# Optimization experiments

Hardware: AMD Instinct MI355X
Metric: run time of the kernel (lower is better)

## Reference

```python
import jax, jax.numpy as jnp
import numpy as np

B, N1, NL, D_MODEL, A, D_K, D_V, D_OUT = 16, 32, 256, 16, 2, 8, 8, 16


def setup_inputs() -> dict:
    key = jax.random.key(0)
    ks = jax.random.split(key, 7)
    he = lambda k, shape, fan_in: jax.random.normal(k, shape, dtype=jnp.float32) * np.sqrt(2.0 / fan_in).astype(np.float32)
    return {
        "Q": jax.random.normal(ks[0], (B, N1, NL, D_MODEL), dtype=jnp.float32),
        "K": jax.random.normal(ks[1], (B, N1, NL, D_MODEL), dtype=jnp.float32),
        "V": jax.random.normal(ks[2], (B, N1, NL, D_MODEL), dtype=jnp.float32),
        "Wq": he(ks[3], (D_MODEL, A, D_K), D_MODEL),
        "Wk": he(ks[4], (D_MODEL, A, D_K), D_MODEL),
        "Wv": he(ks[5], (D_MODEL, A, D_V), D_MODEL),
        "Wo": he(ks[6], (D_V, A, D_OUT), D_V),
    }


def reference(Q, K, V, Wq, Wk, Wv, Wo):
    # Per-head projections: [B, N1, NL, D_k|D_v, A]
    Qp = jnp.einsum('bnki,iaj->bnkja', Q, Wq)
    Kp = jnp.einsum('bnki,iaj->bnkja', K, Wk)
    Vp = jnp.einsum('bnki,iaj->bnkja', V, Wv)
    # Attention maps: [B, N1, NL, NL, A], elementwise ReLU instead of softmax
    attn = jnp.einsum('bnkja,bnzja->bnkza', Qp, Kp)
    attn = jax.nn.relu(attn)
    # Weighted sum of values: [B, N1, NL, D_v, A]
    emb = jnp.einsum('bnkza,bnzma->bnkma', attn, Vp)
    # Output projection mixing heads: [B, N1, NL, D_out]
    proj = jnp.einsum('bnkma,maz->bnkz', emb, Wo)
    # Mean attention map over heads: [B, N1, NL, NL]
    attn_mean = jnp.mean(attn, axis=-1)
    return (proj, attn_mean)
```

## Files before the change

### kernel.cpp

```cpp
#include <hip/hip_runtime.h>

#define B_    16
#define N1_   32
#define NL_   256
#define DM_   16
#define A_    2
#define DK_   8
#define DV_   8
#define DOUT_ 16

#define NBN   (B_ * N1_)
#define PROJ_ELEMS (NBN * NL_ * DOUT_)
#define ZT    32
#define ATP   33

__global__ __launch_bounds__(256, 2)
void mha_relu_kernel(const float* __restrict__ Q,
                     const float* __restrict__ K,
                     const float* __restrict__ V,
                     const float* __restrict__ Wq,
                     const float* __restrict__ Wk,
                     const float* __restrict__ Wv,
                     const float* __restrict__ Wo,
                     float* __restrict__ proj_out,
                     float* __restrict__ attn_out)
{
    __shared__ float sWq[DM_ * A_ * DK_];
    __shared__ float sWk[DM_ * A_ * DK_];
    __shared__ float sWv[DM_ * A_ * DV_];
    __shared__ float sWo[DV_ * A_ * DOUT_];
    __shared__ float KP[NL_ * 16];
    __shared__ float VP[NL_ * 16];
    __shared__ float AT[NL_ * ATP];

    const int tid = threadIdx.x;
    const int bn  = blockIdx.x;
    const int k   = tid;

    sWq[tid] = Wq[tid];
    sWk[tid] = Wk[tid];
    sWv[tid] = Wv[tid];
    sWo[tid] = Wo[tid];
    __syncthreads();

    const size_t inoff = (size_t)bn * NL_ * DM_;

    float Qp[16];
    float rowbuf[16];

    {
        const float4* p = (const float4*)(Q + inoff + (size_t)k * DM_);
        #pragma unroll
        for (int i = 0; i < 4; ++i) {
            float4 t = p[i];
            rowbuf[4*i+0] = t.x; rowbuf[4*i+1] = t.y;
            rowbuf[4*i+2] = t.z; rowbuf[4*i+3] = t.w;
        }
        #pragma unroll
        for (int t = 0; t < 16; ++t) Qp[t] = 0.f;
        #pragma unroll
        for (int i = 0; i < 16; ++i) {
            float qi = rowbuf[i];
            #pragma unroll
            for (int t = 0; t < 16; ++t) Qp[t] += qi * sWq[i*16 + t];
        }
    }
    {
        const float4* p = (const float4*)(K + inoff + (size_t)k * DM_);
        #pragma unroll
        for (int i = 0; i < 4; ++i) {
            float4 t = p[i];
            rowbuf[4*i+0] = t.x; rowbuf[4*i+1] = t.y;
            rowbuf[4*i+2] = t.z; rowbuf[4*i+3] = t.w;
        }
        float acc[16];
        #pragma unroll
        for (int t = 0; t < 16; ++t) acc[t] = 0.f;
        #pragma unroll
        for (int i = 0; i < 16; ++i) {
            float ki = rowbuf[i];
            #pragma unroll
            for (int t = 0; t < 16; ++t) acc[t] += ki * sWk[i*16 + t];
        }
        #pragma unroll
        for (int t = 0; t < 16; ++t) KP[k*16 + t] = acc[t];
    }
    {
        const float4* p = (const float4*)(V + inoff + (size_t)k * DM_);
        #pragma unroll
        for (int i = 0; i < 4; ++i) {
            float4 t = p[i];
            rowbuf[4*i+0] = t.x; rowbuf[4*i+1] = t.y;
            rowbuf[4*i+2] = t.z; rowbuf[4*i+3] = t.w;
        }
        float acc[16];
        #pragma unroll
        for (int t = 0; t < 16; ++t) acc[t] = 0.f;
        #pragma unroll
        for (int i = 0; i < 16; ++i) {
            float vi = rowbuf[i];
            #pragma unroll
            for (int t = 0; t < 16; ++t) acc[t] += vi * sWv[i*16 + t];
        }
        #pragma unroll
        for (int t = 0; t < 16; ++t) VP[k*16 + t] = acc[t];
    }
    __syncthreads();

    float emb[16];
    #pragma unroll
    for (int t = 0; t < 16; ++t) emb[t] = 0.f;

    float* atrow = &AT[k * ATP];
    float* aout  = attn_out + (size_t)bn * NL_ * NL_;

    for (int tile = 0; tile < NL_ / ZT; ++tile) {
        const int z0 = tile * ZT;

        #pragma unroll 8
        for (int zt = 0; zt < ZT; ++zt) {
            const int z = z0 + zt;
            const float4* kpv = (const float4*)&KP[z * 16];
            float kp[16];
            #pragma unroll
            for (int i = 0; i < 4; ++i) {
                float4 t = kpv[i];
                kp[4*i+0] = t.x; kp[4*i+1] = t.y;
                kp[4*i+2] = t.z; kp[4*i+3] = t.w;
            }
            float s0 = 0.f, s1 = 0.f;
            #pragma unroll
            for (int j = 0; j < 8; ++j) {
                s0 += Qp[j]     * kp[j];
                s1 += Qp[8 + j] * kp[8 + j];
            }
            s0 = fmaxf(s0, 0.f);
            s1 = fmaxf(s1, 0.f);
            atrow[zt] = 0.5f * (s0 + s1);

            const float4* vpv = (const float4*)&VP[z * 16];
            float vp[16];
            #pragma unroll
            for (int i = 0; i < 4; ++i) {
                float4 t = vpv[i];
                vp[4*i+0] = t.x; vp[4*i+1] = t.y;
                vp[4*i+2] = t.z; vp[4*i+3] = t.w;
            }
            #pragma unroll
            for (int t = 0; t < 8; ++t) {
                emb[t]     += s0 * vp[t];
                emb[8 + t] += s1 * vp[8 + t];
            }
        }
        __syncthreads();

        #pragma unroll
        for (int i = 0; i < (NL_ * ZT) / 256; ++i) {
            const int idx = i * 256 + tid;
            const int row = idx >> 5;
            const int col = idx & 31;
            aout[(size_t)row * NL_ + z0 + col] = AT[row * ATP + col];
        }
        __syncthreads();
    }

    float pr[16];
    #pragma unroll
    for (int o = 0; o < 16; ++o) pr[o] = 0.f;
    #pragma unroll
    for (int a = 0; a < 2; ++a) {
        #pragma unroll
        for (int m = 0; m < 8; ++m) {
            const float e = emb[a*8 + m];
            #pragma unroll
            for (int o = 0; o < 16; ++o) pr[o] += e * sWo[m*32 + a*16 + o];
        }
    }
    float4* po = (float4*)(proj_out + (size_t)bn * NL_ * DOUT_ + (size_t)k * DOUT_);
    po[0] = make_float4(pr[0],  pr[1],  pr[2],  pr[3]);
    po[1] = make_float4(pr[4],  pr[5],  pr[6],  pr[7]);
    po[2] = make_float4(pr[8],  pr[9],  pr[10], pr[11]);
    po[3] = make_float4(pr[12], pr[13], pr[14], pr[15]);
}

extern "C" void kernel_launch(void* const* d_in, const int* in_sizes, int n_in,
                              void* d_out, int out_size, void* d_ws, size_t ws_size,
                              hipStream_t stream) {
    const float* Q  = (const float*)d_in[0];
    const float* K  = (const float*)d_in[1];
    const float* V  = (const float*)d_in[2];
    const float* Wq = (const float*)d_in[3];
    const float* Wk = (const float*)d_in[4];
    const float* Wv = (const float*)d_in[5];
    const float* Wo = (const float*)d_in[6];

    float* proj = (float*)d_out;
    float* attn = (float*)d_out + PROJ_ELEMS;

    mha_relu_kernel<<<NBN, 256, 0, stream>>>(Q, K, V, Wq, Wk, Wv, Wo, proj, attn);
}
```

Measured before the change: 75.91 us.

## Register-tile four query rows per thread and split key range across waves

Each wave now owns a 64-key slice and each thread computes four query rows, so every K/V row read from LDS is reused four times instead of once. Attention-map values are written straight to global memory as float4, replacing the LDS transpose tile and its per-tile barriers. Partial embeddings from the four waves are reduced through LDS before the output projection. This costs more registers (64 Qp plus 64 emb accumulators per thread) and adds a cross-wave reduction. Each thread's float4 stores now land at addresses a full row apart, so they coalesce less well than before.

```diff
diff --git a/kernel.cpp b/kernel.cpp
--- a/kernel.cpp
+++ b/kernel.cpp
@@ -11,8 +11,17 @@
 
 #define NBN   (B_ * N1_)
 #define PROJ_ELEMS (NBN * NL_ * DOUT_)
-#define ZT    32
-#define ATP   33
+
+#define QP_OFF   0
+#define KP_OFF   4352
+#define VP_OFF   8448
+#define WQ_OFF   12544
+#define WK_OFF   12800
+#define WV_OFF   13056
+#define WO_OFF   13312
+#define LDS_FLOATS 13568
+#define EMBA_OFF 0
+#define EMBB_OFF 4352
 
 __global__ __launch_bounds__(256, 2)
 void mha_relu_kernel(const float* __restrict__ Q,
@@ -25,144 +34,167 @@
                      float* __restrict__ proj_out,
                      float* __restrict__ attn_out)
 {
-    __shared__ float sWq[DM_ * A_ * DK_];
-    __shared__ float sWk[DM_ * A_ * DK_];
-    __shared__ float sWv[DM_ * A_ * DV_];
-    __shared__ float sWo[DV_ * A_ * DOUT_];
-    __shared__ float KP[NL_ * 16];
-    __shared__ float VP[NL_ * 16];
-    __shared__ float AT[NL_ * ATP];
+    __shared__ float lds[LDS_FLOATS];
 
     const int tid = threadIdx.x;
     const int bn  = blockIdx.x;
-    const int k   = tid;
-
-    sWq[tid] = Wq[tid];
-    sWk[tid] = Wk[tid];
-    sWv[tid] = Wv[tid];
-    sWo[tid] = Wo[tid];
+    const int w   = tid >> 6;
+    const int l   = tid & 63;
+
+    lds[WQ_OFF + tid] = Wq[tid];
+    lds[WK_OFF + tid] = Wk[tid];
+    lds[WV_OFF + tid] = Wv[tid];
+    lds[WO_OFF + tid] = Wo[tid];
     __syncthreads();
 
     const size_t inoff = (size_t)bn * NL_ * DM_;
 
-    float Qp[16];
-    float rowbuf[16];
-
     {
-        const float4* p = (const float4*)(Q + inoff + (size_t)k * DM_);
-        #pragma unroll
-        for (int i = 0; i < 4; ++i) {
-            float4 t = p[i];
-            rowbuf[4*i+0] = t.x; rowbuf[4*i+1] = t.y;
-            rowbuf[4*i+2] = t.z; rowbuf[4*i+3] = t.w;
-        }
-        #pragma unroll
-        for (int t = 0; t < 16; ++t) Qp[t] = 0.f;
-        #pragma unroll
-        for (int i = 0; i < 16; ++i) {
-            float qi = rowbuf[i];
-            #pragma unroll
-            for (int t = 0; t < 16; ++t) Qp[t] += qi * sWq[i*16 + t];
-        }
-    }
-    {
-        const float4* p = (const float4*)(K + inoff + (size_t)k * DM_);
-        #pragma unroll
-        for (int i = 0; i < 4; ++i) {
-            float4 t = p[i];
-            rowbuf[4*i+0] = t.x; rowbuf[4*i+1] = t.y;
-            rowbuf[4*i+2] = t.z; rowbuf[4*i+3] = t.w;
-        }
-        float acc[16];
-        #pragma unroll
-        for (int t = 0; t < 16; ++t) acc[t] = 0.f;
-        #pragma unroll
-        for (int i = 0; i < 16; ++i) {
-            float ki = rowbuf[i];
-            #pragma unroll
-            for (int t = 0; t < 16; ++t) acc[t] += ki * sWk[i*16 + t];
-        }
-        #pragma unroll
-        for (int t = 0; t < 16; ++t) KP[k*16 + t] = acc[t];
-    }
-    {
-        const float4* p = (const float4*)(V + inoff + (size_t)k * DM_);
-        #pragma unroll
-        for (int i = 0; i < 4; ++i) {
-            float4 t = p[i];
-            rowbuf[4*i+0] = t.x; rowbuf[4*i+1] = t.y;
-            rowbuf[4*i+2] = t.z; rowbuf[4*i+3] = t.w;
-        }
-        float acc[16];
-        #pragma unroll
-        for (int t = 0; t < 16; ++t) acc[t] = 0.f;
-        #pragma unroll
-        for (int i = 0; i < 16; ++i) {
-            float vi = rowbuf[i];
-            #pragma unroll
-            for (int t = 0; t < 16; ++t) acc[t] += vi * sWv[i*16 + t];
-        }
-        #pragma unroll
-        for (int t = 0; t < 16; ++t) VP[k*16 + t] = acc[t];
-    }
-    __syncthreads();
-
-    float emb[16];
-    #pragma unroll
-    for (int t = 0; t < 16; ++t) emb[t] = 0.f;
-
-    float* atrow = &AT[k * ATP];
-    float* aout  = attn_out + (size_t)bn * NL_ * NL_;
-
-    for (int tile = 0; tile < NL_ / ZT; ++tile) {
-        const int z0 = tile * ZT;
-
-        #pragma unroll 8
-        for (int zt = 0; zt < ZT; ++zt) {
-            const int z = z0 + zt;
-            const float4* kpv = (const float4*)&KP[z * 16];
-            float kp[16];
+        float rowbuf[16], acc[16];
+
+        {
+            const float4* p = (const float4*)(Q + inoff + (size_t)tid * DM_);
             #pragma unroll
             for (int i = 0; i < 4; ++i) {
-                float4 t = kpv[i];
-                kp[4*i+0] = t.x; kp[4*i+1] = t.y;
-                kp[4*i+2] = t.z; kp[4*i+3] = t.w;
-            }
-            float s0 = 0.f, s1 = 0.f;
-            #pragma unroll
-            for (int j = 0; j < 8; ++j) {
-                s0 += Qp[j]     * kp[j];
-                s1 += Qp[8 + j] * kp[8 + j];
-            }
-            s0 = fmaxf(s0, 0.f);
-            s1 = fmaxf(s1, 0.f);
-            atrow[zt] = 0.5f * (s0 + s1);
-
-            const float4* vpv = (const float4*)&VP[z * 16];
-            float vp[16];
+                float4 t = p[i];
+                rowbuf[4*i+0] = t.x; rowbuf[4*i+1] = t.y;
+                rowbuf[4*i+2] = t.z; rowbuf[4*i+3] = t.w;
+            }
+            #pragma unroll
+            for (int c = 0; c < 16; ++c) acc[c] = 0.f;
+            #pragma unroll
+            for (int i = 0; i < 16; ++i) {
+                const float qi = rowbuf[i];
+                #pragma unroll
+                for (int c = 0; c < 16; ++c) acc[c] += qi * lds[WQ_OFF + i*16 + c];
+            }
+            #pragma unroll
+            for (int c = 0; c < 16; ++c) lds[QP_OFF + tid*17 + c] = acc[c];
+        }
+        {
+            const float4* p = (const float4*)(K + inoff + (size_t)tid * DM_);
             #pragma unroll
             for (int i = 0; i < 4; ++i) {
-                float4 t = vpv[i];
-                vp[4*i+0] = t.x; vp[4*i+1] = t.y;
-                vp[4*i+2] = t.z; vp[4*i+3] = t.w;
-            }
-            #pragma unroll
-            for (int t = 0; t < 8; ++t) {
-                emb[t]     += s0 * vp[t];
-                emb[8 + t] += s1 * vp[8 + t];
-            }
-        }
-        __syncthreads();
-
-        #pragma unroll
-        for (int i = 0; i < (NL_ * ZT) / 256; ++i) {
-            const int idx = i * 256 + tid;
-            const int row = idx >> 5;
-            const int col = idx & 31;
-            aout[(size_t)row * NL_ + z0 + col] = AT[row * ATP + col];
-        }
-        __syncthreads();
-    }
+                float4 t = p[i];
+                rowbuf[4*i+0] = t.x; rowbuf[4*i+1] = t.y;
+                rowbuf[4*i+2] = t.z; rowbuf[4*i+3] = t.w;
+            }
+            #pragma unroll
+            for (int c = 0; c < 16; ++c) acc[c] = 0.f;
+            #pragma unroll
+            for (int i = 0; i < 16; ++i) {
+                const float ki = rowbuf[i];
+                #pragma unroll
+                for (int c = 0; c < 16; ++c) acc[c] += ki * lds[WK_OFF + i*16 + c];
+            }
+            #pragma unroll
+            for (int c = 0; c < 16; ++c) lds[KP_OFF + tid*16 + c] = acc[c];
+        }
+        {
+            const float4* p = (const float4*)(V + inoff + (size_t)tid * DM_);
+            #pragma unroll
+            for (int i = 0; i < 4; ++i) {
+                float4 t = p[i];
+                rowbuf[4*i+0] = t.x; rowbuf[4*i+1] = t.y;
+                rowbuf[4*i+2] = t.z; rowbuf[4*i+3] = t.w;
+            }
+            #pragma unroll
+            for (int c = 0; c < 16; ++c) acc[c] = 0.f;
+            #pragma unroll
+            for (int i = 0; i < 16; ++i) {
+                const float vi = rowbuf[i];
+                #pragma unroll
+                for (int c = 0; c < 16; ++c) acc[c] += vi * lds[WV_OFF + i*16 + c];
+            }
+            #pragma unroll
+            for (int c = 0; c < 16; ++c) lds[VP_OFF + tid*16 + c] = acc[c];
+        }
+    }
+    __syncthreads();
+
+    float Qp[4][16];
+    #pragma unroll
+    for (int j = 0; j < 4; ++j) {
+        const int row = 64*j + l;
+        #pragma unroll
+        for (int c = 0; c < 16; ++c) Qp[j][c] = lds[QP_OFF + row*17 + c];
+    }
+
+    float emb[4][16];
+    #pragma unroll
+    for (int j = 0; j < 4; ++j)
+        #pragma unroll
+        for (int c = 0; c < 16; ++c) emb[j][c] = 0.f;
+
+    const int z0 = w * 64;
+    float* aout = attn_out + (size_t)bn * NL_ * NL_;
+
+    #pragma unroll 1
+    for (int zt = 0; zt < 16; ++zt) {
+        float at4[4][4];
+        #pragma unroll
+        for (int dz = 0; dz < 4; ++dz) {
+            const int z = z0 + zt*4 + dz;
+            const float4 k0 = *(const float4*)&lds[KP_OFF + z*16 + 0];
+            const float4 k1 = *(const float4*)&lds[KP_OFF + z*16 + 4];
+            const float4 k2 = *(const float4*)&lds[KP_OFF + z*16 + 8];
+            const float4 k3 = *(const float4*)&lds[KP_OFF + z*16 + 12];
+            const float4 v0 = *(const float4*)&lds[VP_OFF + z*16 + 0];
+            const float4 v1 = *(const float4*)&lds[VP_OFF + z*16 + 4];
+            const float4 v2 = *(const float4*)&lds[VP_OFF + z*16 + 8];
+            const float4 v3 = *(const float4*)&lds[VP_OFF + z*16 + 12];
+            #pragma unroll
+            for (int j = 0; j < 4; ++j) {
+                float s0 = Qp[j][0]*k0.x + Qp[j][1]*k0.y + Qp[j][2]*k0.z + Qp[j][3]*k0.w
+                         + Qp[j][4]*k1.x + Qp[j][5]*k1.y + Qp[j][6]*k1.z + Qp[j][7]*k1.w;
+                float s1 = Qp[j][8]*k2.x + Qp[j][9]*k2.y + Qp[j][10]*k2.z + Qp[j][11]*k2.w
+                         + Qp[j][12]*k3.x + Qp[j][13]*k3.y + Qp[j][14]*k3.z + Qp[j][15]*k3.w;
+                s0 = fmaxf(s0, 0.f);
+                s1 = fmaxf(s1, 0.f);
+                at4[j][dz] = 0.5f * (s0 + s1);
+                emb[j][0]  += s0*v0.x; emb[j][1]  += s0*v0.y; emb[j][2]  += s0*v0.z; emb[j][3]  += s0*v0.w;
+                emb[j][4]  += s0*v1.x; emb[j][5]  += s0*v1.y; emb[j][6]  += s0*v1.z; emb[j][7]  += s0*v1.w;
+                emb[j][8]  += s1*v2.x; emb[j][9]  += s1*v2.y; emb[j][10] += s1*v2.z; emb[j][11] += s1*v2.w;
+                emb[j][12] += s1*v3.x; emb[j][13] += s1*v3.y; emb[j][14] += s1*v3.z; emb[j][15] += s1*v3.w;
+            }
+        }
+        #pragma unroll
+        for (int j = 0; j < 4; ++j) {
+            *(float4*)&aout[(size_t)(64*j + l) * NL_ + z0 + zt*4] =
+                make_float4(at4[j][0], at4[j][1], at4[j][2], at4[j][3]);
+        }
+    }
+
+    __syncthreads();
+    if (w == 0) {
+        #pragma unroll
+        for (int j = 0; j < 4; ++j)
+            #pragma unroll
+            for (int c = 0; c < 16; ++c) lds[EMBA_OFF + (64*j+l)*17 + c] = emb[j][c];
+    } else if (w == 1) {
+        #pragma unroll
+        for (int j = 0; j < 4; ++j)
+            #pragma unroll
+            for (int c = 0; c < 16; ++c) lds[EMBB_OFF + (64*j+l)*17 + c] = emb[j][c];
+    }
+    __syncthreads();
+    if (w == 2) {
+        #pragma unroll
+        for (int j = 0; j < 4; ++j)
+            #pragma unroll
+            for (int c = 0; c < 16; ++c) lds[EMBA_OFF + (64*j+l)*17 + c] += emb[j][c];
+    } else if (w == 3) {
+        #pragma unroll
+        for (int j = 0; j < 4; ++j)
+            #pragma unroll
+            for (int c = 0; c < 16; ++c) lds[EMBB_OFF + (64*j+l)*17 + c] += emb[j][c];
+    }
+    __syncthreads();
+
+    float e[16];
+    #pragma unroll
+    for (int c = 0; c < 16; ++c)
+        e[c] = lds[EMBA_OFF + tid*17 + c] + lds[EMBB_OFF + tid*17 + c];
 
     float pr[16];
     #pragma unroll
@@ -171,12 +203,12 @@
     for (int a = 0; a < 2; ++a) {
         #pragma unroll
         for (int m = 0; m < 8; ++m) {
-            const float e = emb[a*8 + m];
-            #pragma unroll
-            for (int o = 0; o < 16; ++o) pr[o] += e * sWo[m*32 + a*16 + o];
-        }
-    }
-    float4* po = (float4*)(proj_out + (size_t)bn * NL_ * DOUT_ + (size_t)k * DOUT_);
+            const float ev = e[a*8 + m];
+            #pragma unroll
+            for (int o = 0; o < 16; ++o) pr[o] += ev * lds[WO_OFF + m*32 + a*16 + o];
+        }
+    }
+    float4* po = (float4*)(proj_out + (size_t)bn * NL_ * DOUT_ + (size_t)tid * DOUT_);
     po[0] = make_float4(pr[0],  pr[1],  pr[2],  pr[3]);
     po[1] = make_float4(pr[4],  pr[5],  pr[6],  pr[7]);
     po[2] = make_float4(pr[8],  pr[9],  pr[10], pr[11]);
```

Result: slower. 137.7 us (+81.4%).
